# Optimization experiments

Measured on AMD Instinct MI355X. Metric: run time of the kernel, lower is better.

The kernel has to match this reference:

```python
import jax, jax.numpy as jnp
import numpy as np

VOCAB, E, H, OUT = 24, 16, 32, 2
B, T = 16384, 128


def setup_inputs() -> dict:
    key = jax.random.key(0)
    ks = jax.random.split(key, 8)
    x = jax.random.randint(ks[0], (B, T), 0, VOCAB, dtype=jnp.int32)
    emb = jax.random.normal(ks[1], (VOCAB, E), dtype=jnp.float32) * 0.1
    emb = emb.at[0].set(0.0)  # padding_idx=0
    s = 1.0 / np.sqrt(H)
    W_ih = jax.random.uniform(ks[2], (4 * H, E), minval=-s, maxval=s, dtype=jnp.float32)
    W_hh = jax.random.uniform(ks[3], (4 * H, H), minval=-s, maxval=s, dtype=jnp.float32)
    b_ih = jax.random.uniform(ks[4], (4 * H,), minval=-s, maxval=s, dtype=jnp.float32)
    b_hh = jax.random.uniform(ks[5], (4 * H,), minval=-s, maxval=s, dtype=jnp.float32)
    sf = 1.0 / np.sqrt(H)
    fc_w = jax.random.uniform(ks[6], (OUT, H), minval=-sf, maxval=sf, dtype=jnp.float32)
    fc_b = jax.random.uniform(ks[7], (OUT,), minval=-sf, maxval=sf, dtype=jnp.float32)
    return {"x": x, "emb": emb, "W_ih": W_ih, "W_hh": W_hh,
            "b_ih": b_ih, "b_hh": b_hh, "fc_w": fc_w, "fc_b": fc_b}


def _lstm_last_h(xe, W_ih, W_hh, b_ih, b_hh):
    # xe: [B, T, E]. PyTorch gate order: i, f, g, o.
    b = xe.shape[0]
    # Precompute input projections for all timesteps in one GEMM: [B, T, 4H]
    gates_x = jnp.einsum('bte,ge->btg', xe, W_ih) + (b_ih + b_hh)

    def step(carry, gx_t):
        h, c = carry
        gates = gx_t + h @ W_hh.T  # [B, 4H]
        i, f, g, o = jnp.split(gates, 4, axis=-1)
        i = jax.nn.sigmoid(i)
        f = jax.nn.sigmoid(f)
        g = jnp.tanh(g)
        o = jax.nn.sigmoid(o)
        c = f * c + i * g
        h = o * jnp.tanh(c)
        return (h, c), None

    h0 = jnp.zeros((b, W_hh.shape[1]), dtype=xe.dtype)
    c0 = jnp.zeros_like(h0)
    (h_last, _), _ = jax.lax.scan(step, (h0, c0), jnp.swapaxes(gates_x, 0, 1))
    return h_last  # == lstm_outputs[:, -1, :]


def reference(x, emb, W_ih, W_hh, b_ih, b_hh, fc_w, fc_b):
    xe = emb[x]                                   # [B, T, E] embedding lookup
    h_last = _lstm_last_h(xe, W_ih, W_hh, b_ih, b_hh)  # [B, H]
    return h_last @ fc_w.T + fc_b                 # [B, 2]
```

## Files before the change

### kernel.cpp

```cpp
#include <hip/hip_runtime.h>
#include <hip/hip_bf16.h>

typedef __bf16 bf16x8 __attribute__((ext_vector_type(8)));
typedef float  f32x4  __attribute__((ext_vector_type(4)));

#define VOCAB 24
#define EDIM  16
#define HDIM  32
#define TLEN  128

union A2U { int4 w; bf16x8 v; };

__device__ __forceinline__ float xor8f(float v) {
    int r = __builtin_amdgcn_update_dpp(0, __float_as_int(v), 0x128, 0xF, 0xF, true);
    return __int_as_float(r);
}
__device__ __forceinline__ float rsig(float a) {
    return __builtin_amdgcn_rcpf(1.0f + __builtin_amdgcn_exp2f(a));
}
__device__ __forceinline__ float fast_tanh(float x) {
    float t = __builtin_amdgcn_exp2f(x * -2.88539008f);
    return fmaf(2.0f, __builtin_amdgcn_rcpf(1.0f + t), -1.0f);
}

__global__ __launch_bounds__(256, 2) void lstm_fused(
    const int*   __restrict__ x,
    const float* __restrict__ emb,
    const float* __restrict__ W_ih,
    const float* __restrict__ W_hh,
    const float* __restrict__ b_ih,
    const float* __restrict__ b_hh,
    const float* __restrict__ fc_w,
    const float* __restrict__ fc_b,
    float*       __restrict__ out)
{
    __shared__ __align__(16) __bf16 hbuf[2][32][40];
    __shared__ __align__(16) float  fbuf[32][33];

    const int tid   = threadIdx.x;
    const int wid   = tid >> 6;
    const int lane  = tid & 63;
    const int l15   = lane & 15;
    const int hi    = lane >> 4;
    const int kbase = hi * 8;
    const int kh    = hi * 4;
    const int row0  = blockIdx.x * 32;
    const bool lowj = (l15 < 8);
    const int  j    = wid * 8 + (l15 & 7);

    bf16x8 b1f[2];
    bf16x8 b2f[2];
    #pragma unroll
    for (int p = 0; p < 2; ++p) {
        const int q    = 2 * p + (l15 >> 3);
        const int gcol = q * 32 + j;
        const float scale = (q == 2) ? -2.88539008f : -1.44269504f;
        const float* wrow = W_hh + gcol * HDIM;
        #pragma unroll
        for (int i = 0; i < 8; ++i)
            b1f[p][i] = (__bf16)(scale * wrow[kbase + i]);
        const float bias = b_ih[gcol] + b_hh[gcol];
        const float* wi = W_ih + gcol * EDIM;
        #pragma unroll
        for (int i = 0; i < 8; ++i) {
            const int v = kbase + i;
            float s = 0.0f;
            if (v < VOCAB) {
                s = bias;
                #pragma unroll
                for (int e = 0; e < EDIM; ++e)
                    s += emb[v * EDIM + e] * wi[e];
            }
            b2f[p][i] = (__bf16)(scale * s);
        }
    }

    const float a1c  = lowj ?  2.0f : 1.0f;
    const float b1c  = lowj ? -1.0f : 0.0f;
    const int   urow = 4 * hi + (lowj ? 0 : 2);

    float cA0 = 0.0f, cA1 = 0.0f, cB0 = 0.0f, cB1 = 0.0f;
    const int* xrowA = x + (row0 + l15) * TLEN;
    const int* xrowB = xrowA + 16 * TLEN;
    const f32x4 z = {0.f, 0.f, 0.f, 0.f};

    int4 xqA = *(const int4*)xrowA;
    int4 xqB = *(const int4*)xrowB;

#define ONEHOT(DST, XV) do {                                                   \
    const int xv_   = (XV);                                                    \
    const int hotw_ = 0x3F80 << ((xv_ & 1) << 4);                              \
    const int hoth_ = xv_ >> 1;                                                \
    DST.w.x = (hoth_ == kh + 0) ? hotw_ : 0;                                   \
    DST.w.y = (hoth_ == kh + 1) ? hotw_ : 0;                                   \
    DST.w.z = (hoth_ == kh + 2) ? hotw_ : 0;                                   \
    DST.w.w = (hoth_ == kh + 3) ? hotw_ : 0;                                   \
} while (0)

#define GUPD(A0, A1, C0, C1, HV0, HV1) do {                                    \
    const float s00_ = rsig(A0[0]), s01_ = rsig(A0[1]);                        \
    const float s02_ = rsig(A0[2]), s03_ = rsig(A0[3]);                        \
    const float s10_ = fmaf(a1c, rsig(A1[0]), b1c);                            \
    const float s11_ = fmaf(a1c, rsig(A1[1]), b1c);                            \
    const float s12_ = fmaf(a1c, rsig(A1[2]), b1c);                            \
    const float s13_ = fmaf(a1c, rsig(A1[3]), b1c);                            \
    const float x00_ = xor8f(s00_), x01_ = xor8f(s01_);                        \
    const float x02_ = xor8f(s02_), x03_ = xor8f(s03_);                        \
    const float x10_ = xor8f(s10_), x11_ = xor8f(s11_);                        \
    const float x12_ = xor8f(s12_), x13_ = xor8f(s13_);                        \
    const float iv0_ = lowj ? s00_ : x02_;                                     \
    const float fv0_ = lowj ? x00_ : s02_;                                     \
    const float gv0_ = lowj ? s10_ : x12_;                                     \
    const float ov0_ = lowj ? x10_ : s12_;                                     \
    C0 = fmaf(fv0_, C0, iv0_ * gv0_);                                          \
    HV0 = ov0_ * fast_tanh(C0);                                                \
    const float iv1_ = lowj ? s01_ : x03_;                                     \
    const float fv1_ = lowj ? x01_ : s03_;                                     \
    const float gv1_ = lowj ? s11_ : x13_;                                     \
    const float ov1_ = lowj ? x11_ : s13_;                                     \
    C1 = fmaf(fv1_, C1, iv1_ * gv1_);                                          \
    HV1 = ov1_ * fast_tanh(C1);                                                \
} while (0)

#define SLOT(XVA, XVB, P, FIRST, LAST) do {                                    \
    A2U a2A_, a2B_;                                                            \
    ONEHOT(a2A_, XVA);                                                         \
    ONEHOT(a2B_, XVB);                                                         \
    f32x4 aA0_ = __builtin_amdgcn_mfma_f32_16x16x32_bf16(a2A_.v, b2f[0], z, 0, 0, 0); \
    f32x4 aA1_ = __builtin_amdgcn_mfma_f32_16x16x32_bf16(a2A_.v, b2f[1], z, 0, 0, 0); \
    f32x4 aB0_ = __builtin_amdgcn_mfma_f32_16x16x32_bf16(a2B_.v, b2f[0], z, 0, 0, 0); \
    f32x4 aB1_ = __builtin_amdgcn_mfma_f32_16x16x32_bf16(a2B_.v, b2f[1], z, 0, 0, 0); \
    if (!(FIRST)) {                                                            \
        const bf16x8 a1A_ = *(const bf16x8*)&hbuf[(P) ^ 1][l15     ][kbase];   \
        const bf16x8 a1B_ = *(const bf16x8*)&hbuf[(P) ^ 1][l15 + 16][kbase];   \
        aA0_ = __builtin_amdgcn_mfma_f32_16x16x32_bf16(a1A_, b1f[0], aA0_, 0, 0, 0); \
        aA1_ = __builtin_amdgcn_mfma_f32_16x16x32_bf16(a1A_, b1f[1], aA1_, 0, 0, 0); \
        aB0_ = __builtin_amdgcn_mfma_f32_16x16x32_bf16(a1B_, b1f[0], aB0_, 0, 0, 0); \
        aB1_ = __builtin_amdgcn_mfma_f32_16x16x32_bf16(a1B_, b1f[1], aB1_, 0, 0, 0); \
    }                                                                          \
    float hA0_, hA1_, hB0_, hB1_;                                              \
    GUPD(aA0_, aA1_, cA0, cA1, hA0_, hA1_);                                    \
    GUPD(aB0_, aB1_, cB0, cB1, hB0_, hB1_);                                    \
    if (!(LAST)) {                                                             \
        hbuf[P][urow         ][j] = (__bf16)hA0_;                              \
        hbuf[P][urow + 1     ][j] = (__bf16)hA1_;                              \
        hbuf[P][urow + 16    ][j] = (__bf16)hB0_;                              \
        hbuf[P][urow + 17    ][j] = (__bf16)hB1_;                              \
    } else {                                                                   \
        fbuf[urow     ][j] = hA0_;                                             \
        fbuf[urow + 1 ][j] = hA1_;                                             \
        fbuf[urow + 16][j] = hB0_;                                             \
        fbuf[urow + 17][j] = hB1_;                                             \
    }                                                                          \
    __syncthreads();                                                           \
} while (0)

    SLOT(xqA.x, xqB.x, 0, true, false);

    #pragma unroll 1
    for (int t = 1; t < 125; t += 4) {
        SLOT(xqA.y, xqB.y, 1, false, false);
        SLOT(xqA.z, xqB.z, 0, false, false);
        SLOT(xqA.w, xqB.w, 1, false, false);
        xqA = *(const int4*)(xrowA + t + 3);
        xqB = *(const int4*)(xrowB + t + 3);
        SLOT(xqA.x, xqB.x, 0, false, false);
    }

    SLOT(xqA.y, xqB.y, 1, false, false);
    SLOT(xqA.z, xqB.z, 0, false, false);
    SLOT(xqA.w, xqB.w, 1, false, true);

#undef SLOT
#undef GUPD
#undef ONEHOT

    if (tid < 32) {
        float o0 = fc_b[0], o1 = fc_b[1];
        #pragma unroll
        for (int jj = 0; jj < HDIM; ++jj) {
            const float h = fbuf[tid][jj];
            o0 += fc_w[jj]        * h;
            o1 += fc_w[HDIM + jj] * h;
        }
        float2 res;
        res.x = o0; res.y = o1;
        *(float2*)&out[(row0 + tid) * 2] = res;
    }
}

extern "C" void kernel_launch(void* const* d_in, const int* in_sizes, int n_in,
                              void* d_out, int out_size, void* d_ws, size_t ws_size,
                              hipStream_t stream) {
    const int*   x    = (const int*)  d_in[0];
    const float* emb  = (const float*)d_in[1];
    const float* W_ih = (const float*)d_in[2];
    const float* W_hh = (const float*)d_in[3];
    const float* b_ih = (const float*)d_in[4];
    const float* b_hh = (const float*)d_in[5];
    const float* fc_w = (const float*)d_in[6];
    const float* fc_b = (const float*)d_in[7];
    float* out = (float*)d_out;

    const int B    = in_sizes[0] / TLEN;
    const int nblk = B / 32;

    lstm_fused<<<nblk, 256, 0, stream>>>(x, emb, W_ih, W_hh, b_ih, b_hh, fc_w, fc_b, out);
}
```

Measured before the change: 120.7 us.

## Software-pipeline input-projection MFMAs for next timestep ahead of the barrier

Moves the one-hot embedding-projection MFMAs for timestep t+1 to right after the h writes of step t, before the barrier. They now overlap with barrier wait time instead of sitting on the recurrent critical path. The barrier moves to the start of each slot, and the token loads are prefetched one loop iteration earlier. This costs extra live accumulator registers and restructures the prologue and epilogue slot counts.

```diff
diff --git a/kernel.cpp b/kernel.cpp
--- a/kernel.cpp
+++ b/kernel.cpp
@@ -84,8 +84,7 @@
     const int* xrowB = xrowA + 16 * TLEN;
     const f32x4 z = {0.f, 0.f, 0.f, 0.f};
 
-    int4 xqA = *(const int4*)xrowA;
-    int4 xqB = *(const int4*)xrowB;
+    f32x4 pA0, pA1, pB0, pB1;
 
 #define ONEHOT(DST, XV) do {                                                   \
     const int xv_   = (XV);                                                    \
@@ -95,6 +94,16 @@
     DST.w.y = (hoth_ == kh + 1) ? hotw_ : 0;                                   \
     DST.w.z = (hoth_ == kh + 2) ? hotw_ : 0;                                   \
     DST.w.w = (hoth_ == kh + 3) ? hotw_ : 0;                                   \
+} while (0)
+
+#define PRECOMP(XVA, XVB) do {                                                 \
+    A2U a2A_, a2B_;                                                            \
+    ONEHOT(a2A_, XVA);                                                         \
+    ONEHOT(a2B_, XVB);                                                         \
+    pA0 = __builtin_amdgcn_mfma_f32_16x16x32_bf16(a2A_.v, b2f[0], z, 0, 0, 0); \
+    pA1 = __builtin_amdgcn_mfma_f32_16x16x32_bf16(a2A_.v, b2f[1], z, 0, 0, 0); \
+    pB0 = __builtin_amdgcn_mfma_f32_16x16x32_bf16(a2B_.v, b2f[0], z, 0, 0, 0); \
+    pB1 = __builtin_amdgcn_mfma_f32_16x16x32_bf16(a2B_.v, b2f[1], z, 0, 0, 0); \
 } while (0)
 
 #define GUPD(A0, A1, C0, C1, HV0, HV1) do {                                    \
@@ -122,58 +131,69 @@
     HV1 = ov1_ * fast_tanh(C1);                                                \
 } while (0)
 
-#define SLOT(XVA, XVB, P, FIRST, LAST) do {                                    \
-    A2U a2A_, a2B_;                                                            \
-    ONEHOT(a2A_, XVA);                                                         \
-    ONEHOT(a2B_, XVB);                                                         \
-    f32x4 aA0_ = __builtin_amdgcn_mfma_f32_16x16x32_bf16(a2A_.v, b2f[0], z, 0, 0, 0); \
-    f32x4 aA1_ = __builtin_amdgcn_mfma_f32_16x16x32_bf16(a2A_.v, b2f[1], z, 0, 0, 0); \
-    f32x4 aB0_ = __builtin_amdgcn_mfma_f32_16x16x32_bf16(a2B_.v, b2f[0], z, 0, 0, 0); \
-    f32x4 aB1_ = __builtin_amdgcn_mfma_f32_16x16x32_bf16(a2B_.v, b2f[1], z, 0, 0, 0); \
-    if (!(FIRST)) {                                                            \
+#define SLOT(P, FIRST, LAST, XVNA, XVNB) do {                                  \
+    f32x4 aA0_, aA1_, aB0_, aB1_;                                              \
+    if (FIRST) {                                                               \
+        aA0_ = pA0; aA1_ = pA1; aB0_ = pB0; aB1_ = pB1;                        \
+    } else {                                                                   \
+        __syncthreads();                                                       \
         const bf16x8 a1A_ = *(const bf16x8*)&hbuf[(P) ^ 1][l15     ][kbase];   \
         const bf16x8 a1B_ = *(const bf16x8*)&hbuf[(P) ^ 1][l15 + 16][kbase];   \
-        aA0_ = __builtin_amdgcn_mfma_f32_16x16x32_bf16(a1A_, b1f[0], aA0_, 0, 0, 0); \
-        aA1_ = __builtin_amdgcn_mfma_f32_16x16x32_bf16(a1A_, b1f[1], aA1_, 0, 0, 0); \
-        aB0_ = __builtin_amdgcn_mfma_f32_16x16x32_bf16(a1B_, b1f[0], aB0_, 0, 0, 0); \
-        aB1_ = __builtin_amdgcn_mfma_f32_16x16x32_bf16(a1B_, b1f[1], aB1_, 0, 0, 0); \
+        aA0_ = __builtin_amdgcn_mfma_f32_16x16x32_bf16(a1A_, b1f[0], pA0, 0, 0, 0); \
+        aA1_ = __builtin_amdgcn_mfma_f32_16x16x32_bf16(a1A_, b1f[1], pA1, 0, 0, 0); \
+        aB0_ = __builtin_amdgcn_mfma_f32_16x16x32_bf16(a1B_, b1f[0], pB0, 0, 0, 0); \
+        aB1_ = __builtin_amdgcn_mfma_f32_16x16x32_bf16(a1B_, b1f[1], pB1, 0, 0, 0); \
     }                                                                          \
     float hA0_, hA1_, hB0_, hB1_;                                              \
     GUPD(aA0_, aA1_, cA0, cA1, hA0_, hA1_);                                    \
     GUPD(aB0_, aB1_, cB0, cB1, hB0_, hB1_);                                    \
     if (!(LAST)) {                                                             \
-        hbuf[P][urow         ][j] = (__bf16)hA0_;                              \
-        hbuf[P][urow + 1     ][j] = (__bf16)hA1_;                              \
-        hbuf[P][urow + 16    ][j] = (__bf16)hB0_;                              \
-        hbuf[P][urow + 17    ][j] = (__bf16)hB1_;                              \
+        hbuf[P][urow     ][j] = (__bf16)hA0_;                                  \
+        hbuf[P][urow + 1 ][j] = (__bf16)hA1_;                                  \
+        hbuf[P][urow + 16][j] = (__bf16)hB0_;                                  \
+        hbuf[P][urow + 17][j] = (__bf16)hB1_;                                  \
+        PRECOMP(XVNA, XVNB);                                                   \
     } else {                                                                   \
         fbuf[urow     ][j] = hA0_;                                             \
         fbuf[urow + 1 ][j] = hA1_;                                             \
         fbuf[urow + 16][j] = hB0_;                                             \
         fbuf[urow + 17][j] = hB1_;                                             \
     }                                                                          \
-    __syncthreads();                                                           \
-} while (0)
-
-    SLOT(xqA.x, xqB.x, 0, true, false);
+} while (0)
+
+    int4 q0A = *(const int4*)xrowA;
+    int4 q0B = *(const int4*)xrowB;
+    int4 xqA = *(const int4*)(xrowA + 4);
+    int4 xqB = *(const int4*)(xrowB + 4);
+    PRECOMP(q0A.x, q0B.x);
+
+    SLOT(0, true,  false, q0A.y, q0B.y);
+    SLOT(1, false, false, q0A.z, q0B.z);
+    SLOT(0, false, false, q0A.w, q0B.w);
 
     #pragma unroll 1
-    for (int t = 1; t < 125; t += 4) {
-        SLOT(xqA.y, xqB.y, 1, false, false);
-        SLOT(xqA.z, xqB.z, 0, false, false);
-        SLOT(xqA.w, xqB.w, 1, false, false);
-        xqA = *(const int4*)(xrowA + t + 3);
-        xqB = *(const int4*)(xrowB + t + 3);
-        SLOT(xqA.x, xqB.x, 0, false, false);
+    for (int t = 3; t < 123; t += 4) {
+        const int4 nA = *(const int4*)(xrowA + t + 5);
+        const int4 nB = *(const int4*)(xrowB + t + 5);
+        SLOT(1, false, false, xqA.x, xqB.x);
+        SLOT(0, false, false, xqA.y, xqB.y);
+        SLOT(1, false, false, xqA.z, xqB.z);
+        SLOT(0, false, false, xqA.w, xqB.w);
+        xqA = nA; xqB = nB;
     }
 
-    SLOT(xqA.y, xqB.y, 1, false, false);
-    SLOT(xqA.z, xqB.z, 0, false, false);
-    SLOT(xqA.w, xqB.w, 1, false, true);
+    SLOT(1, false, false, xqA.x, xqB.x);
+    SLOT(0, false, false, xqA.y, xqB.y);
+    SLOT(1, false, false, xqA.z, xqB.z);
+    SLOT(0, false, false, xqA.w, xqB.w);
+    SLOT(1, false, true,  0,     0);
 
 #undef SLOT
 #undef GUPD
+#undef PRECOMP
 #undef ONEHOT
+
+    __syncthreads();
 
     if (tid < 32) {
         float o0 = fc_b[0], o1 = fc_b[1];
```

Result: no change. 118.4 us (-1.9%).
